# Optimization experiments

Measured on AMD Instinct MI355X. Metric: run time of the kernel, lower is better.

Reference implementation:

```python
import jax, jax.numpy as jnp
import numpy as np

GAMMA = 1.0          # smoothing parameter (init default)
NORMALIZE = False    # init default
BIG = 1e10           # finite stand-in for +inf boundary (exp(-BIG/gamma) == 0, grad-safe)


def setup_inputs() -> dict:
    key = jax.random.key(0)
    k1, k2 = jax.random.split(key)
    B, T, D = 64, 1024, 8
    pred = jax.random.normal(k1, (B, T, D), dtype=jnp.float32)
    target = jax.random.normal(k2, (B, T, D), dtype=jnp.float32)
    return {"pred": pred, "target": target}


def _soft_dtw(dist, gamma):
    # dist: [B, T, T] pairwise squared distances. Returns R[:, -1, -1] of shape [B].
    B, T, _ = dist.shape
    inv_g = 1.0 / gamma

    def inner_step(r_left, inp):
        # r_left = R[i, j-1]; r0 = R[i-1, j-1]; r1 = R[i-1, j]; d = D[i-1, j-1]
        r0, r1, d = inp  # each [B]
        stack = jnp.stack([r0, r1, r_left], axis=-1)          # [B, 3]
        rmin = -gamma * jax.nn.logsumexp(-stack * inv_g, axis=-1)
        val = d + rmin
        return val, val

    def outer_step(prev_row, d_row):
        # prev_row: [B, T+1] = R[i-1, :]; d_row: [B, T] = D[i-1, :]
        xs = (prev_row[:, :-1].T, prev_row[:, 1:].T, d_row.T)  # each [T, B]
        r_init = jnp.full((B,), BIG, dist.dtype)               # R[i, 0] = inf
        _, vals = jax.lax.scan(inner_step, r_init, xs)         # vals: [T, B]
        new_row = jnp.concatenate(
            [jnp.full((B, 1), BIG, dist.dtype), vals.T], axis=1)  # [B, T+1]
        return new_row, None

    # R[0, 0] = 0, R[0, j>0] = inf
    row0 = jnp.concatenate(
        [jnp.zeros((B, 1), dist.dtype), jnp.full((B, T), BIG, dist.dtype)], axis=1)
    last_row, _ = jax.lax.scan(outer_step, row0, jnp.transpose(dist, (1, 0, 2)))
    return last_row[:, -1]  # R[:, T, T]


def reference(pred, target):
    B, T, D = pred.shape
    # [B, T, T] squared Euclidean distance between all time-step pairs
    dist = jnp.sum((pred[:, :, None, :] - target[:, None, :, :]) ** 2, axis=-1)
    loss = _soft_dtw(dist, GAMMA)  # [B]
    if NORMALIZE:
        loss = loss / T
    return jnp.mean(loss)
```

## Files before the change

kernel.cpp:

```cpp
#include <hip/hip_runtime.h>


typedef float v2f __attribute__((ext_vector_type(2)));

static constexpr int T      = 1024;
static constexpr int NB     = 64;
static constexpr int NTH    = 512;
static constexpr int NW     = 8;
static constexpr int CT     = 2;
static constexpr int NQ     = T / CT;
static constexpr int WSTEPS = NQ + 63;

#define BIGF 1e10f
#define L2EF 1.4426950408889634f
#define LN2F 0.6931471805599453f

__device__ __forceinline__ float fexp2(float x) { return __builtin_amdgcn_exp2f(x); }
__device__ __forceinline__ float flog2(float x) { return __builtin_amdgcn_logf(x); }

__device__ __forceinline__ float softmin2(float a, float b, float c) {
  float m = fminf(fminf(a, b), c);
  float M = fmaxf(fmaxf(a, b), c);
  float e = __builtin_amdgcn_fmed3f(a, b, c);
  float s = fexp2(m - e) + fexp2(m - M);
  return m - flog2(1.0f + s);
}

__device__ __forceinline__ v2f pkfma(v2f a, v2f b, v2f c) {
  v2f d;
  asm("v_pk_fma_f32 %0, %1, %2, %3" : "=v"(d) : "v"(a), "v"(b), "v"(c));
  return d;
}

__device__ __forceinline__ v2f lo2(const float4& c) { v2f r; r.x = c.x; r.y = c.y; return r; }
__device__ __forceinline__ v2f hi2(const float4& c) { v2f r; r.x = c.z; r.y = c.w; return r; }

__device__ __forceinline__ v2f dotpk(v2f seed, const v2f* pp, const float4* C) {
  v2f a = seed;
  a = pkfma(pp[0], lo2(C[0]), a);
  a = pkfma(pp[1], hi2(C[0]), a);
  a = pkfma(pp[2], lo2(C[1]), a);
  a = pkfma(pp[3], hi2(C[1]), a);
  a = pkfma(pp[4], lo2(C[2]), a);
  a = pkfma(pp[5], hi2(C[2]), a);
  a = pkfma(pp[6], lo2(C[3]), a);
  a = pkfma(pp[7], hi2(C[3]), a);
  return a;
}

#define STEP(SW, CUR, CN, NXT, NN)                                           \
  {                                                                          \
    const int sw_ = (SW);                                                    \
    float2 cb = make_float2(BIGF, BIGF);                                     \
    if (w > 0 && sw_ < NQ) {                                                 \
      if ((sw_ & 3) == 0) {                                                  \
        const int need = ((sw_ + 3 < NQ) ? sw_ + 3 : NQ - 1) + 63;           \
        while (seen < need) {                                                 \
          seen = __hip_atomic_load(&prog_s[w - 1], __ATOMIC_ACQUIRE,         \
                                   __HIP_MEMORY_SCOPE_WORKGROUP);            \
          if (seen < need) __builtin_amdgcn_s_sleep(1);                      \
        }                                                                    \
      }                                                                      \
      cb = buf_s[(w - 1) * NQ + sw_];       \
    }                                                                        \
    float na0 = __shfl_up(v10, 1, 64);                                       \
    float na1 = __shfl_up(v11, 1, 64);                                       \
    float a0 = (lane == 0) ? cb.x : na0;                                     \
    float a1 = (lane == 0) ? cb.y : na1;                                     \
    const int q = sw_ - lane;                                                \
    {            \
      int qn = sw_ + 1 - lane;                                               \
      qn = qn < 0 ? 0 : (qn > NQ - 1 ? NQ - 1 : qn);                         \
      const float4* bp = &tgt4_s[qn * 4];                                    \
      NXT[0] = bp[0]; NXT[1] = bp[1]; NXT[2] = bp[2]; NXT[3] = bp[3];        \
      NN = tn2_s[qn];                                                        \
    }                                                                        \
    if (q >= 0 && q < NQ) {                                                  \
      v2f seedA; seedA.x = pn0 + CN.x; seedA.y = pn0 + CN.y;                 \
      v2f seedB; seedB.x = pn1 + CN.x; seedB.y = pn1 + CN.y;                 \
      v2f accA = dotpk(seedA, pApk, CUR);                                    \
      v2f accB = dotpk(seedB, pBpk, CUR);                                    \
      float v00 = accA.x + softmin2(carry, a0, l0);                          \
      float v01 = accA.y + softmin2(a0, a1, v00);                            \
      v10 = accB.x + softmin2(l0, v00, l1);                                  \
      v11 = accB.y + softmin2(v00, v01, v10);                                \
      l0 = v01; l1 = v11; carry = a1;                                        \
      if (lane == 63 && w < NW - 1)                                          \
        buf_s[w * NQ + q] = make_float2(v10, v11);                           \
      if (t == NTH - 1 && q == NQ - 1) ws[b] = v11 * LN2F;                   \
    }                                                                        \
    if (lane == 63 && w < NW - 1 && ((sw_ & 3) == 3 || sw_ == WSTEPS - 1))   \
      __hip_atomic_store(&prog_s[w], sw_, __ATOMIC_RELEASE,                  \
                         __HIP_MEMORY_SCOPE_WORKGROUP);                      \
  }

__global__ __launch_bounds__(NTH) void sdtw_kernel(const float* __restrict__ pred,
                                                   const float* __restrict__ target,
                                                   float* __restrict__ ws) {
  __shared__ float4 tgt4_s[NQ * 4];
  __shared__ float2 tn2_s[NQ];
  __shared__ float2 buf_s[(NW - 1) * NQ];
  __shared__ int prog_s[NW];

  const int t    = threadIdx.x;
  const int w    = t >> 6;
  const int lane = t & 63;
  const int b    = blockIdx.x;
  const float* pr = pred + (size_t)b * T * 8;
  const float* tg = target + (size_t)b * T * 8;

  {
    const float4* tg4 = reinterpret_cast<const float4*>(tg);
    float4 v0 = tg4[t * 4 + 0];
    float4 v1 = tg4[t * 4 + 1];
    float4 v2 = tg4[t * 4 + 2];
    float4 v3 = tg4[t * 4 + 3];
    float tn0 = (v0.x * v0.x + v0.y * v0.y) + (v0.z * v0.z + v0.w * v0.w) +
                (v1.x * v1.x + v1.y * v1.y) + (v1.z * v1.z + v1.w * v1.w);
    float tn1 = (v2.x * v2.x + v2.y * v2.y) + (v2.z * v2.z + v2.w * v2.w) +
                (v3.x * v3.x + v3.y * v3.y) + (v3.z * v3.z + v3.w * v3.w);
    const float s = -2.0f * L2EF;
    tgt4_s[t * 4 + 0] = make_float4(v0.x * s, v2.x * s, v0.y * s, v2.y * s);
    tgt4_s[t * 4 + 1] = make_float4(v0.z * s, v2.z * s, v0.w * s, v2.w * s);
    tgt4_s[t * 4 + 2] = make_float4(v1.x * s, v3.x * s, v1.y * s, v3.y * s);
    tgt4_s[t * 4 + 3] = make_float4(v1.z * s, v3.z * s, v1.w * s, v3.w * s);
    tn2_s[t] = make_float2(tn0 * L2EF, tn1 * L2EF);
  }
  if (t < NW) prog_s[t] = -1;

  const float4* pr4 = reinterpret_cast<const float4*>(pr);
  float4 pA0 = pr4[t * 4 + 0];
  float4 pA1 = pr4[t * 4 + 1];
  float4 pB0 = pr4[t * 4 + 2];
  float4 pB1 = pr4[t * 4 + 3];
  float pn0 = ((pA0.x * pA0.x + pA0.y * pA0.y) + (pA0.z * pA0.z + pA0.w * pA0.w) +
               (pA1.x * pA1.x + pA1.y * pA1.y) + (pA1.z * pA1.z + pA1.w * pA1.w)) * L2EF;
  float pn1 = ((pB0.x * pB0.x + pB0.y * pB0.y) + (pB0.z * pB0.z + pB0.w * pB0.w) +
               (pB1.x * pB1.x + pB1.y * pB1.y) + (pB1.z * pB1.z + pB1.w * pB1.w)) * L2EF;
  v2f pApk[8], pBpk[8];
  pApk[0].x = pA0.x; pApk[0].y = pA0.x;  pApk[1].x = pA0.y; pApk[1].y = pA0.y;
  pApk[2].x = pA0.z; pApk[2].y = pA0.z;  pApk[3].x = pA0.w; pApk[3].y = pA0.w;
  pApk[4].x = pA1.x; pApk[4].y = pA1.x;  pApk[5].x = pA1.y; pApk[5].y = pA1.y;
  pApk[6].x = pA1.z; pApk[6].y = pA1.z;  pApk[7].x = pA1.w; pApk[7].y = pA1.w;
  pBpk[0].x = pB0.x; pBpk[0].y = pB0.x;  pBpk[1].x = pB0.y; pBpk[1].y = pB0.y;
  pBpk[2].x = pB0.z; pBpk[2].y = pB0.z;  pBpk[3].x = pB0.w; pBpk[3].y = pB0.w;
  pBpk[4].x = pB1.x; pBpk[4].y = pB1.x;  pBpk[5].x = pB1.y; pBpk[5].y = pB1.y;
  pBpk[6].x = pB1.z; pBpk[6].y = pB1.z;  pBpk[7].x = pB1.w; pBpk[7].y = pB1.w;

  __syncthreads();

  float l0 = BIGF, l1 = BIGF;
  float carry = (t == 0) ? 0.0f : BIGF;
  float v10 = BIGF, v11 = BIGF;
  int seen = -1;

  float4 tgA[4], tgB[4];
  float2 tnA, tnB;
  {
    tgA[0] = tgt4_s[0]; tgA[1] = tgt4_s[1]; tgA[2] = tgt4_s[2]; tgA[3] = tgt4_s[3];
    tnA = tn2_s[0];
  }

  for (int sw = 0; sw < 576; sw += 2) {
    STEP(sw, tgA, tnA, tgB, tnB)
    STEP(sw + 1, tgB, tnB, tgA, tnA)
  }
}

__global__ void sdtw_reduce(const float* __restrict__ ws, float* __restrict__ out) {
  int l = threadIdx.x;
  float v = ws[l];
#pragma unroll
  for (int k = 32; k >= 1; k >>= 1) v += __shfl_down(v, k, 64);
  if (l == 0) out[0] = v * (1.0f / (float)NB);
}

extern "C" void kernel_launch(void* const* d_in, const int* in_sizes, int n_in,
                              void* d_out, int out_size, void* d_ws, size_t ws_size,
                              hipStream_t stream) {
  const float* pred   = (const float*)d_in[0];
  const float* target = (const float*)d_in[1];
  float* out = (float*)d_out;
  float* ws  = (float*)d_ws;

  sdtw_kernel<<<NB, NTH, 0, stream>>>(pred, target, ws);
  sdtw_reduce<<<1, 64, 0, stream>>>(ws, out);
}
```

Baseline: 448.8 us.

## Process four pred rows per thread with half the waves, pack target norms

Each thread now computes four consecutive pred rows instead of two, so the block shrinks to 4 waves of 256 threads. This halves the number of inter-wave pipeline hand-offs and their fill latency. The cost is a longer serial softmin dependency chain in each anti-diagonal step, which now runs eight softmins instead of four. The target squared norms are also folded into a fifth float4 per target pair in shared memory, so the separate norm array and its separate LDS load go away.

```diff
diff --git a/kernel.cpp b/kernel.cpp
--- a/kernel.cpp
+++ b/kernel.cpp
@@ -5,8 +5,8 @@
 
 static constexpr int T      = 1024;
 static constexpr int NB     = 64;
-static constexpr int NTH    = 512;
-static constexpr int NW     = 8;
+static constexpr int NTH    = 256;
+static constexpr int NW     = 4;
 static constexpr int CT     = 2;
 static constexpr int NQ     = T / CT;
 static constexpr int WSTEPS = NQ + 63;
@@ -48,7 +48,7 @@
   return a;
 }
 
-#define STEP(SW, CUR, CN, NXT, NN)                                           \
+#define STEP(SW, CUR, NXT)                                                   \
   {                                                                          \
     const int sw_ = (SW);                                                    \
     float2 cb = make_float2(BIGF, BIGF);                                     \
@@ -63,31 +63,40 @@
       }                                                                      \
       cb = buf_s[(w - 1) * NQ + sw_];       \
     }                                                                        \
-    float na0 = __shfl_up(v10, 1, 64);                                       \
-    float na1 = __shfl_up(v11, 1, 64);                                       \
+    float na0 = __shfl_up(vD0, 1, 64);                                       \
+    float na1 = __shfl_up(vD1, 1, 64);                                       \
     float a0 = (lane == 0) ? cb.x : na0;                                     \
     float a1 = (lane == 0) ? cb.y : na1;                                     \
     const int q = sw_ - lane;                                                \
     {            \
       int qn = sw_ + 1 - lane;                                               \
       qn = qn < 0 ? 0 : (qn > NQ - 1 ? NQ - 1 : qn);                         \
-      const float4* bp = &tgt4_s[qn * 4];                                    \
+      const float4* bp = &tgt4_s[qn * 5];                                    \
       NXT[0] = bp[0]; NXT[1] = bp[1]; NXT[2] = bp[2]; NXT[3] = bp[3];        \
-      NN = tn2_s[qn];                                                        \
+      NXT[4] = bp[4];                                                        \
     }                                                                        \
     if (q >= 0 && q < NQ) {                                                  \
-      v2f seedA; seedA.x = pn0 + CN.x; seedA.y = pn0 + CN.y;                 \
-      v2f seedB; seedB.x = pn1 + CN.x; seedB.y = pn1 + CN.y;                 \
-      v2f accA = dotpk(seedA, pApk, CUR);                                    \
-      v2f accB = dotpk(seedB, pBpk, CUR);                                    \
-      float v00 = accA.x + softmin2(carry, a0, l0);                          \
-      float v01 = accA.y + softmin2(a0, a1, v00);                            \
-      v10 = accB.x + softmin2(l0, v00, l1);                                  \
-      v11 = accB.y + softmin2(v00, v01, v10);                                \
-      l0 = v01; l1 = v11; carry = a1;                                        \
+      const float tn0 = CUR[4].x, tn1 = CUR[4].y;                            \
+      v2f sA; sA.x = pnA + tn0; sA.y = pnA + tn1;                            \
+      v2f sB; sB.x = pnB + tn0; sB.y = pnB + tn1;                            \
+      v2f sC; sC.x = pnC + tn0; sC.y = pnC + tn1;                            \
+      v2f sD; sD.x = pnD + tn0; sD.y = pnD + tn1;                            \
+      v2f accA = dotpk(sA, ppA, CUR);                                        \
+      v2f accB = dotpk(sB, ppB, CUR);                                        \
+      v2f accC = dotpk(sC, ppC, CUR);                                        \
+      v2f accD = dotpk(sD, ppD, CUR);                                        \
+      float vA0 = accA.x + softmin2(carry, a0, lA);                          \
+      float vA1 = accA.y + softmin2(a0, a1, vA0);                            \
+      float vB0 = accB.x + softmin2(lA, vA0, lB);                            \
+      float vB1 = accB.y + softmin2(vA0, vA1, vB0);                          \
+      float vC0 = accC.x + softmin2(lB, vB0, lC);                            \
+      float vC1 = accC.y + softmin2(vB0, vB1, vC0);                          \
+      vD0 = accD.x + softmin2(lC, vC0, lD);                                  \
+      vD1 = accD.y + softmin2(vC0, vC1, vD0);                                \
+      lA = vA1; lB = vB1; lC = vC1; lD = vD1; carry = a1;                    \
       if (lane == 63 && w < NW - 1)                                          \
-        buf_s[w * NQ + q] = make_float2(v10, v11);                           \
-      if (t == NTH - 1 && q == NQ - 1) ws[b] = v11 * LN2F;                   \
+        buf_s[w * NQ + q] = make_float2(vD0, vD1);                           \
+      if (t == NTH - 1 && q == NQ - 1) ws[b] = vD1 * LN2F;                   \
     }                                                                        \
     if (lane == 63 && w < NW - 1 && ((sw_ & 3) == 3 || sw_ == WSTEPS - 1))   \
       __hip_atomic_store(&prog_s[w], sw_, __ATOMIC_RELEASE,                  \
@@ -97,8 +106,7 @@
 __global__ __launch_bounds__(NTH) void sdtw_kernel(const float* __restrict__ pred,
                                                    const float* __restrict__ target,
                                                    float* __restrict__ ws) {
-  __shared__ float4 tgt4_s[NQ * 4];
-  __shared__ float2 tn2_s[NQ];
+  __shared__ float4 tgt4_s[NQ * 5];
   __shared__ float2 buf_s[(NW - 1) * NQ];
   __shared__ int prog_s[NW];
 
@@ -111,59 +119,61 @@
 
   {
     const float4* tg4 = reinterpret_cast<const float4*>(tg);
-    float4 v0 = tg4[t * 4 + 0];
-    float4 v1 = tg4[t * 4 + 1];
-    float4 v2 = tg4[t * 4 + 2];
-    float4 v3 = tg4[t * 4 + 3];
-    float tn0 = (v0.x * v0.x + v0.y * v0.y) + (v0.z * v0.z + v0.w * v0.w) +
-                (v1.x * v1.x + v1.y * v1.y) + (v1.z * v1.z + v1.w * v1.w);
-    float tn1 = (v2.x * v2.x + v2.y * v2.y) + (v2.z * v2.z + v2.w * v2.w) +
-                (v3.x * v3.x + v3.y * v3.y) + (v3.z * v3.z + v3.w * v3.w);
     const float s = -2.0f * L2EF;
-    tgt4_s[t * 4 + 0] = make_float4(v0.x * s, v2.x * s, v0.y * s, v2.y * s);
-    tgt4_s[t * 4 + 1] = make_float4(v0.z * s, v2.z * s, v0.w * s, v2.w * s);
-    tgt4_s[t * 4 + 2] = make_float4(v1.x * s, v3.x * s, v1.y * s, v3.y * s);
-    tgt4_s[t * 4 + 3] = make_float4(v1.z * s, v3.z * s, v1.w * s, v3.w * s);
-    tn2_s[t] = make_float2(tn0 * L2EF, tn1 * L2EF);
+#pragma unroll
+    for (int h = 0; h < 2; ++h) {
+      float4 u0 = tg4[t * 8 + 4 * h + 0];
+      float4 u1 = tg4[t * 8 + 4 * h + 1];
+      float4 u2 = tg4[t * 8 + 4 * h + 2];
+      float4 u3 = tg4[t * 8 + 4 * h + 3];
+      float tA = (u0.x * u0.x + u0.y * u0.y) + (u0.z * u0.z + u0.w * u0.w) +
+                 (u1.x * u1.x + u1.y * u1.y) + (u1.z * u1.z + u1.w * u1.w);
+      float tB = (u2.x * u2.x + u2.y * u2.y) + (u2.z * u2.z + u2.w * u2.w) +
+                 (u3.x * u3.x + u3.y * u3.y) + (u3.z * u3.z + u3.w * u3.w);
+      float4* dst = &tgt4_s[(2 * t + h) * 5];
+      dst[0] = make_float4(u0.x * s, u2.x * s, u0.y * s, u2.y * s);
+      dst[1] = make_float4(u0.z * s, u2.z * s, u0.w * s, u2.w * s);
+      dst[2] = make_float4(u1.x * s, u3.x * s, u1.y * s, u3.y * s);
+      dst[3] = make_float4(u1.z * s, u3.z * s, u1.w * s, u3.w * s);
+      dst[4] = make_float4(tA * L2EF, tB * L2EF, 0.0f, 0.0f);
+    }
   }
   if (t < NW) prog_s[t] = -1;
 
   const float4* pr4 = reinterpret_cast<const float4*>(pr);
-  float4 pA0 = pr4[t * 4 + 0];
-  float4 pA1 = pr4[t * 4 + 1];
-  float4 pB0 = pr4[t * 4 + 2];
-  float4 pB1 = pr4[t * 4 + 3];
-  float pn0 = ((pA0.x * pA0.x + pA0.y * pA0.y) + (pA0.z * pA0.z + pA0.w * pA0.w) +
-               (pA1.x * pA1.x + pA1.y * pA1.y) + (pA1.z * pA1.z + pA1.w * pA1.w)) * L2EF;
-  float pn1 = ((pB0.x * pB0.x + pB0.y * pB0.y) + (pB0.z * pB0.z + pB0.w * pB0.w) +
-               (pB1.x * pB1.x + pB1.y * pB1.y) + (pB1.z * pB1.z + pB1.w * pB1.w)) * L2EF;
-  v2f pApk[8], pBpk[8];
-  pApk[0].x = pA0.x; pApk[0].y = pA0.x;  pApk[1].x = pA0.y; pApk[1].y = pA0.y;
-  pApk[2].x = pA0.z; pApk[2].y = pA0.z;  pApk[3].x = pA0.w; pApk[3].y = pA0.w;
-  pApk[4].x = pA1.x; pApk[4].y = pA1.x;  pApk[5].x = pA1.y; pApk[5].y = pA1.y;
-  pApk[6].x = pA1.z; pApk[6].y = pA1.z;  pApk[7].x = pA1.w; pApk[7].y = pA1.w;
-  pBpk[0].x = pB0.x; pBpk[0].y = pB0.x;  pBpk[1].x = pB0.y; pBpk[1].y = pB0.y;
-  pBpk[2].x = pB0.z; pBpk[2].y = pB0.z;  pBpk[3].x = pB0.w; pBpk[3].y = pB0.w;
-  pBpk[4].x = pB1.x; pBpk[4].y = pB1.x;  pBpk[5].x = pB1.y; pBpk[5].y = pB1.y;
-  pBpk[6].x = pB1.z; pBpk[6].y = pB1.z;  pBpk[7].x = pB1.w; pBpk[7].y = pB1.w;
+  float4 qA0 = pr4[t * 8 + 0], qA1 = pr4[t * 8 + 1];
+  float4 qB0 = pr4[t * 8 + 2], qB1 = pr4[t * 8 + 3];
+  float4 qC0 = pr4[t * 8 + 4], qC1 = pr4[t * 8 + 5];
+  float4 qD0 = pr4[t * 8 + 6], qD1 = pr4[t * 8 + 7];
+#define NRM(a, b)                                                            \
+  (((a.x * a.x + a.y * a.y) + (a.z * a.z + a.w * a.w) +                      \
+    (b.x * b.x + b.y * b.y) + (b.z * b.z + b.w * b.w)) * L2EF)
+  float pnA = NRM(qA0, qA1), pnB = NRM(qB0, qB1);
+  float pnC = NRM(qC0, qC1), pnD = NRM(qD0, qD1);
+#define DUP(pp, r0, r1)                                                      \
+  pp[0].x = r0.x; pp[0].y = r0.x; pp[1].x = r0.y; pp[1].y = r0.y;            \
+  pp[2].x = r0.z; pp[2].y = r0.z; pp[3].x = r0.w; pp[3].y = r0.w;            \
+  pp[4].x = r1.x; pp[4].y = r1.x; pp[5].x = r1.y; pp[5].y = r1.y;            \
+  pp[6].x = r1.z; pp[6].y = r1.z; pp[7].x = r1.w; pp[7].y = r1.w;
+  v2f ppA[8], ppB[8], ppC[8], ppD[8];
+  DUP(ppA, qA0, qA1) DUP(ppB, qB0, qB1) DUP(ppC, qC0, qC1) DUP(ppD, qD0, qD1)
 
   __syncthreads();
 
-  float l0 = BIGF, l1 = BIGF;
+  float lA = BIGF, lB = BIGF, lC = BIGF, lD = BIGF;
   float carry = (t == 0) ? 0.0f : BIGF;
-  float v10 = BIGF, v11 = BIGF;
+  float vD0 = BIGF, vD1 = BIGF;
   int seen = -1;
 
-  float4 tgA[4], tgB[4];
-  float2 tnA, tnB;
+  float4 tgA[5], tgB[5];
   {
-    tgA[0] = tgt4_s[0]; tgA[1] = tgt4_s[1]; tgA[2] = tgt4_s[2]; tgA[3] = tgt4_s[3];
-    tnA = tn2_s[0];
+    tgA[0] = tgt4_s[0]; tgA[1] = tgt4_s[1]; tgA[2] = tgt4_s[2];
+    tgA[3] = tgt4_s[3]; tgA[4] = tgt4_s[4];
   }
 
   for (int sw = 0; sw < 576; sw += 2) {
-    STEP(sw, tgA, tnA, tgB, tnB)
-    STEP(sw + 1, tgB, tnB, tgA, tnA)
+    STEP(sw, tgA, tgB)
+    STEP(sw + 1, tgB, tgA)
   }
 }
 
```

Measured after the change: 404.0 us. 1.11x faster.
